# Optimization experiments

Measured on AMD Instinct MI355X. Metric: run time of the kernel, lower is better.

Reference implementation:

```python
import jax, jax.numpy as jnp
import numpy as np

B, S, DIM = 2, 2048, 2048
NH, HD, HDR = 16, 128, 64
DCKV, DCQ = 512, 1536


def _lin(x, W, b):
    return x @ W.T + b


def _rotate_half(x):
    x1, x2 = jnp.split(x, 2, axis=-1)
    return jnp.concatenate([-x2, x1], axis=-1)


def _rope(x, cos, sin):
    # x: [..., s, hdr]; cos/sin: [s, hdr]
    return x * cos + _rotate_half(x) * sin


def setup_inputs() -> dict:
    key = jax.random.key(0)
    ks = jax.random.split(key, 20)
    sc = 0.02

    def w(k, shape):
        return (jax.random.normal(k, shape, jnp.float32) * sc)

    inp = {}
    inp['x'] = jax.random.normal(ks[0], (B, S, DIM), jnp.float32)
    # standard RoPE tables for the decoupled rotary dim
    inv_freq = 1.0 / (10000.0 ** (jnp.arange(0, HDR, 2, dtype=jnp.float32) / HDR))
    t = jnp.arange(S, dtype=jnp.float32)
    freqs = jnp.outer(t, inv_freq)                      # [S, HDR/2]
    emb = jnp.concatenate([freqs, freqs], axis=-1)      # [S, HDR]
    inp['freq_cos'] = jnp.cos(emb)
    inp['freq_sin'] = jnp.sin(emb)
    inp['W_dq'] = w(ks[1], (DCQ, DIM));  inp['b_dq'] = jnp.zeros((DCQ,), jnp.float32)
    inp['W_uq'] = w(ks[2], (NH * HD, DCQ)); inp['b_uq'] = jnp.zeros((NH * HD,), jnp.float32)
    inp['W_qr'] = w(ks[3], (NH * HDR, DCQ)); inp['b_qr'] = jnp.zeros((NH * HDR,), jnp.float32)
    inp['W_dkv'] = w(ks[4], (DCKV, DIM)); inp['b_dkv'] = jnp.zeros((DCKV,), jnp.float32)
    inp['W_uk'] = w(ks[5], (NH * HD, DCKV)); inp['b_uk'] = jnp.zeros((NH * HD,), jnp.float32)
    inp['W_uv'] = w(ks[6], (NH * HD, DCKV)); inp['b_uv'] = jnp.zeros((NH * HD,), jnp.float32)
    inp['W_kr'] = w(ks[7], (HDR, DIM)); inp['b_kr'] = jnp.zeros((HDR,), jnp.float32)
    inp['W_out'] = w(ks[8], (DIM, DIM)); inp['b_out'] = jnp.zeros((DIM,), jnp.float32)
    return inp


def reference(x, freq_cos, freq_sin,
              W_dq, b_dq, W_uq, b_uq, W_qr, b_qr,
              W_dkv, b_dkv, W_uk, b_uk, W_uv, b_uv,
              W_kr, b_kr, W_out, b_out):
    b, s, d = x.shape
    c_q = _lin(x, W_dq, b_dq)                                  # [b,s,dcq]
    c_kv = _lin(x, W_dkv, b_dkv)                               # [b,s,dckv]
    c_q_r = _lin(c_q, W_qr, b_qr).reshape(b, s, NH, HDR).transpose(0, 2, 1, 3)  # [b,nh,s,hdr]
    k_r = _lin(x, W_kr, b_kr)[:, None]                         # [b,1,s,hdr]
    cos = freq_cos[:s]
    sin = freq_sin[:s]
    r_q = _rope(c_q_r, cos, sin)
    r_k = _rope(k_r, cos, sin)
    r_q = r_q.transpose(0, 2, 1, 3).reshape(b, s, NH * HDR)    # [b,s,nh*hdr]
    r_k = r_k[:, 0]                                            # [b,s,hdr]
    q = jnp.concatenate([_lin(c_q, W_uq, b_uq), r_q], axis=-1)  # [b,s,nh*hd+nh*hdr]
    k_base = _lin(c_kv, W_uk, b_uk)                            # [b,s,nh*hd]
    v = _lin(c_kv, W_uv, b_uv)                                 # [b,s,nh*hd]
    r_k_exp = jnp.broadcast_to(r_k[:, :, None, :], (b, s, NH, HDR)).reshape(b, s, NH * HDR)
    k = jnp.concatenate([k_base, r_k_exp], axis=-1)
    # faithful to original: view the concat into nh chunks of (hd+hdr)
    q = q.reshape(b, s, NH, HD + HDR).transpose(0, 2, 1, 3)    # [b,nh,s,hd+hdr]
    k = k.reshape(b, s, NH, HD + HDR).transpose(0, 2, 1, 3)
    v = v.reshape(b, s, NH, HD).transpose(0, 2, 1, 3)          # [b,nh,s,hd]
    scale = 1.0 / np.float32(np.sqrt(HD + HDR))
    att = jnp.einsum('bhqd,bhkd->bhqk', q, k) * scale          # [b,nh,s,s]
    mask = jnp.tril(jnp.ones((s, s), dtype=bool))
    att = jnp.where(mask, att, jnp.float32(-jnp.inf))
    att = jax.nn.softmax(att, axis=-1)
    y = jnp.einsum('bhqk,bhkd->bhqd', att, v)                  # [b,nh,s,hd]
    y = y.transpose(0, 2, 1, 3).reshape(b, s, d)
    return _lin(y, W_out, b_out)
```

## Files before the change

kernel.cpp:

```cpp
#include <hip/hip_runtime.h>
#include <hip/hip_bf16.h>
#include <stdint.h>


typedef __bf16 bf16x8 __attribute__((ext_vector_type(8)));
typedef float  f32x4  __attribute__((ext_vector_type(4)));

__device__ __forceinline__ uint16_t f2bf(float f) {
    uint32_t u = __builtin_bit_cast(uint32_t, f);
    u = (u + 0x7FFFu + ((u >> 16) & 1u)) >> 16;
    return (uint16_t)u;
}
__device__ __forceinline__ float bf2f(uint16_t h) {
    uint32_t u = ((uint32_t)h) << 16;
    return __builtin_bit_cast(float, u);
}

typedef __attribute__((address_space(3))) uint32_t lds_u32_t;
typedef const __attribute__((address_space(1))) uint32_t glb_u32_t;

__device__ __forceinline__ void gld16(const void* g, const void* l) {
    __builtin_amdgcn_global_load_lds((glb_u32_t*)(uintptr_t)g,
                                     (lds_u32_t*)(uint32_t)(uintptr_t)l, 16, 0, 0);
}

__global__ __launch_bounds__(256)
void conv_kernel(const float* __restrict__ src, uint16_t* __restrict__ dst,
                 int n_src, int n_dst)
{
    int i = (blockIdx.x * 256 + threadIdx.x) << 2;
    if (i >= n_dst) return;
    ushort4 o;
    if (i < n_src) {
        float4 v = *(const float4*)(src + i);
        o.x = f2bf(v.x); o.y = f2bf(v.y); o.z = f2bf(v.z); o.w = f2bf(v.w);
    } else {
        o.x = 0; o.y = 0; o.z = 0; o.w = 0;
    }
    *(ushort4*)(dst + i) = o;
}

template<int MODE>
__global__ __launch_bounds__(256, 2)
void gemm_fused(const uint16_t* __restrict__ A, const uint16_t* __restrict__ W,
                const float* __restrict__ b0, const float* __restrict__ b1,
                const float* __restrict__ b2,
                void* __restrict__ O0, void* __restrict__ O1,
                int M, int N, int K, int lda, int s1, int s2)
{
    __shared__ __align__(16) uint16_t Alds[128 * 32];
    __shared__ __align__(16) uint16_t Blds[128 * 32];

    const int tid  = threadIdx.x;
    const int lane = tid & 63;
    const int wave = tid >> 6;
    const int wm   = wave >> 1;
    const int wn   = wave & 1;
    const int m0   = blockIdx.y << 7;
    const int n0   = blockIdx.x << 7;

    f32x4 acc[4][4];
    #pragma unroll
    for (int i = 0; i < 4; ++i)
        #pragma unroll
        for (int j = 0; j < 4; ++j)
            acc[i][j] = (f32x4){0.f, 0.f, 0.f, 0.f};

    const int r0 = (wave << 5) + (lane >> 2);
    const int ck = (lane & 3) << 3;
    const uint16_t* gA0 = A + (size_t)(m0 + r0) * lda + ck;
    const uint16_t* gA1 = gA0 + (size_t)16 * lda;
    const uint16_t* gB0 = W + (size_t)(n0 + r0) * K + ck;
    const uint16_t* gB1 = gB0 + (size_t)16 * K;
    const uint16_t* lA0 = Alds + (wave << 10);
    const uint16_t* lA1 = lA0 + 512;
    const uint16_t* lB0 = Blds + (wave << 10);
    const uint16_t* lB1 = lB0 + 512;

    const int rsel = lane & 15;
    const int g8   = (lane >> 4) << 3;

    const int nK = K >> 5;
    for (int kt = 0; kt < nK; ++kt) {
        __syncthreads();
        gld16(gA0, lA0); gld16(gA1, lA1);
        gld16(gB0, lB0); gld16(gB1, lB1);
        gA0 += 32; gA1 += 32; gB0 += 32; gB1 += 32;
        __syncthreads();

        bf16x8 af[4], bfr[4];
        #pragma unroll
        for (int i = 0; i < 4; ++i)
            af[i] = *(const bf16x8*)&Alds[(((wm << 6) + (i << 4) + rsel) << 5) + g8];
        #pragma unroll
        for (int j = 0; j < 4; ++j)
            bfr[j] = *(const bf16x8*)&Blds[(((wn << 6) + (j << 4) + rsel) << 5) + g8];

        #pragma unroll
        for (int i = 0; i < 4; ++i)
            #pragma unroll
            for (int j = 0; j < 4; ++j)
                acc[i][j] = __builtin_amdgcn_mfma_f32_16x16x32_bf16(af[i], bfr[j], acc[i][j], 0, 0, 0);
    }

    const int col = lane & 15;
    const int rg  = lane >> 4;
    #pragma unroll
    for (int i = 0; i < 4; ++i) {
        #pragma unroll
        for (int j = 0; j < 4; ++j) {
            int n = n0 + (wn << 6) + (j << 4) + col;
            if (n >= N) continue;
            float bv = (n < s1) ? b0[n] : (n < s2) ? b1[n - s1] : b2[n - s2];
            float v[4];
            #pragma unroll
            for (int r = 0; r < 4; ++r) v[r] = acc[i][j][r] + bv;
            int mbase = m0 + (wm << 6) + (i << 4) + (rg << 2);
            if (MODE == 0) {
                uint16_t* o = (uint16_t*)O0 + (size_t)mbase * N + n;
                #pragma unroll
                for (int r = 0; r < 4; ++r) o[(size_t)r * N] = f2bf(v[r]);
            } else if (MODE == 3) {
                float* o = (float*)O0 + (size_t)mbase * N + n;
                #pragma unroll
                for (int r = 0; r < 4; ++r) o[(size_t)r * N] = v[r];
            } else {
                if (n < s1) {
                    int hh = n / 192, d = n - hh * 192;
                    int b = mbase >> 11, s = mbase & 2047;
                    uint16_t* o = (uint16_t*)O0 + (((size_t)(b * 16 + hh) * 2048 + s) * 192) + d;
                    #pragma unroll
                    for (int r = 0; r < 4; ++r) o[r * 192] = f2bf(v[r]);
                } else if (MODE == 4) {
                    int nn = n - s1;
                    uint16_t* o = (uint16_t*)O1 + (size_t)mbase * (N - s1) + nn;
                    #pragma unroll
                    for (int r = 0; r < 4; ++r) o[(size_t)r * (N - s1)] = f2bf(v[r]);
                } else {
                    int nn = n - s1;
                    int hh = nn >> 7, d = nn & 127;
                    int b = mbase >> 11, s = mbase & 2047;
                    ushort4 o4;
                    o4.x = f2bf(v[0]); o4.y = f2bf(v[1]); o4.z = f2bf(v[2]); o4.w = f2bf(v[3]);
                    *(ushort4*)&((uint16_t*)O1)[(((size_t)(b * 16 + hh) * 128 + d) * 2048) + s] = o4;
                }
            }
        }
    }
}

__global__ __launch_bounds__(256)
void rope_q_kernel(const uint16_t* __restrict__ raw, const float* __restrict__ fc,
                   const float* __restrict__ fs, uint16_t* __restrict__ qp)
{
    int gid = blockIdx.x * 256 + threadIdx.x;
    int m = gid >> 10, n = gid & 1023;
    int hh = n >> 6, d = n & 63;
    int b = m >> 11, s = m & 2047;
    float x  = bf2f(raw[(size_t)m * 1024 + n]);
    float xo = bf2f(raw[(size_t)m * 1024 + hh * 64 + ((d < 32) ? d + 32 : d - 32)]);
    float rot = (d < 32) ? -xo : xo;
    float v = x * fc[s * 64 + d] + rot * fs[s * 64 + d];
    int f = 2048 + n;
    int head = f / 192, dq = f - head * 192;
    qp[(((size_t)(b * 16 + head) * 2048 + s) * 192) + dq] = f2bf(v);
}

__global__ __launch_bounds__(256)
void rope_k_kernel(const uint16_t* __restrict__ raw, int ldr,
                   const float* __restrict__ fc, const float* __restrict__ fs,
                   uint16_t* __restrict__ kp)
{
    int gid = blockIdx.x * 256 + threadIdx.x;
    int m = gid >> 6, d = gid & 63;
    int b = m >> 11, s = m & 2047;
    float x  = bf2f(raw[(size_t)m * ldr + d]);
    float xo = bf2f(raw[(size_t)m * ldr + ((d < 32) ? d + 32 : d - 32)]);
    float rot = (d < 32) ? -xo : xo;
    uint16_t bv = f2bf(x * fc[s * 64 + d] + rot * fs[s * 64 + d]);
    #pragma unroll
    for (int hh = 0; hh < 16; ++hh) {
        int f = 2048 + hh * 64 + d;
        int head = f / 192, dk = f - head * 192;
        kp[(((size_t)(b * 16 + head) * 2048 + s) * 192) + dk] = bv;
    }
}

__global__ __launch_bounds__(256)
void attn_mfma3(const uint16_t* __restrict__ qp, const uint16_t* __restrict__ kp,
                const uint16_t* __restrict__ vt, uint16_t* __restrict__ yf)
{
    __shared__ uint16_t Ks[64][200];
    __shared__ uint16_t Vs[128][72];
    __shared__ uint16_t Ps[4][16][72];

    const int tid  = threadIdx.x;
    const int lane = tid & 63;
    const int w    = tid >> 6;
    const int g    = lane >> 4;
    const int li   = lane & 15;
    const int bh   = blockIdx.y;
    const int b    = bh >> 4;
    const int h    = bh & 15;

    const size_t qkb = (size_t)bh * 2048 * 192;
    const size_t vtb = (size_t)bh * 128 * 2048;
    const float scl = 0.07216878364870323f * 1.4426950408889634f;

    for (int pass = 0; pass < 2; ++pass) {
        const int jq = pass ? (int)blockIdx.x : 31 - (int)blockIdx.x;
        const int q0 = jq << 6;

        bf16x8 qf[6];
        #pragma unroll
        for (int kk = 0; kk < 6; ++kk)
            qf[kk] = *(const bf16x8*)(qp + qkb +
                (size_t)(q0 + (w << 4) + li) * 192 + kk * 32 + (g << 3));

        float mst[4], lst[4];
        f32x4 oacc[8];
        #pragma unroll
        for (int r = 0; r < 4; ++r) { mst[r] = -__builtin_inff(); lst[r] = 0.f; }
        #pragma unroll
        for (int ct = 0; ct < 8; ++ct) oacc[ct] = (f32x4){0.f, 0.f, 0.f, 0.f};

        for (int t = 0; t <= jq; ++t) {
            const int j0 = t << 6;
            __syncthreads();
            #pragma unroll
            for (int p = 0; p < 6; ++p) {
                int idx = tid + p * 256;
                int r = idx / 24, c8 = (idx - r * 24) << 3;
                *(bf16x8*)&Ks[r][c8] = *(const bf16x8*)(kp + qkb + (size_t)(j0 + r) * 192 + c8);
            }
            #pragma unroll
            for (int p = 0; p < 8; ++p) {
                int idx = tid + p * 256;
                int r = idx >> 4, c4 = (idx & 15) << 2;
                *(ushort4*)&Vs[r][c4] = *(const ushort4*)(vt + vtb + (size_t)r * 2048 + j0 + c4);
            }
            __syncthreads();

            f32x4 sacc[4];
            #pragma unroll
            for (int c = 0; c < 4; ++c) sacc[c] = (f32x4){0.f, 0.f, 0.f, 0.f};
            #pragma unroll
            for (int c = 0; c < 4; ++c) {
                #pragma unroll
                for (int kk = 0; kk < 6; ++kk) {
                    bf16x8 kf = *(const bf16x8*)&Ks[(c << 4) + li][kk * 32 + (g << 3)];
                    sacc[c] = __builtin_amdgcn_mfma_f32_16x16x32_bf16(qf[kk], kf, sacc[c], 0, 0, 0);
                }
            }

            float corr[4];
            #pragma unroll
            for (int r = 0; r < 4; ++r) {
                const int rq = q0 + (w << 4) + (g << 2) + r;
                float sv[4];
                float mx = -__builtin_inff();
                #pragma unroll
                for (int c = 0; c < 4; ++c) {
                    int colk = j0 + (c << 4) + li;
                    sv[c] = (colk <= rq) ? sacc[c][r] * scl : -__builtin_inff();
                    mx = fmaxf(mx, sv[c]);
                }
                #pragma unroll
                for (int off = 8; off >= 1; off >>= 1) mx = fmaxf(mx, __shfl_xor(mx, off, 64));
                float mnew = fmaxf(mst[r], mx);
                corr[r] = exp2f(mst[r] - mnew);
                mst[r] = mnew;
                float psum = 0.f;
                #pragma unroll
                for (int c = 0; c < 4; ++c) {
                    float p = exp2f(sv[c] - mnew);
                    psum += p;
                    Ps[w][(g << 2) + r][(c << 4) + li] = f2bf(p);
                }
                #pragma unroll
                for (int off = 8; off >= 1; off >>= 1) psum += __shfl_xor(psum, off, 64);
                lst[r] = lst[r] * corr[r] + psum;
            }

            #pragma unroll
            for (int ct = 0; ct < 8; ++ct)
                #pragma unroll
                for (int r = 0; r < 4; ++r) oacc[ct][r] *= corr[r];

            bf16x8 pf0 = *(const bf16x8*)&Ps[w][li][(g << 3)];
            bf16x8 pf1 = *(const bf16x8*)&Ps[w][li][32 + (g << 3)];
            #pragma unroll
            for (int ct = 0; ct < 8; ++ct) {
                bf16x8 vf0 = *(const bf16x8*)&Vs[(ct << 4) + li][(g << 3)];
                bf16x8 vf1 = *(const bf16x8*)&Vs[(ct << 4) + li][32 + (g << 3)];
                oacc[ct] = __builtin_amdgcn_mfma_f32_16x16x32_bf16(pf0, vf0, oacc[ct], 0, 0, 0);
                oacc[ct] = __builtin_amdgcn_mfma_f32_16x16x32_bf16(pf1, vf1, oacc[ct], 0, 0, 0);
            }
        }

        #pragma unroll
        for (int r = 0; r < 4; ++r) {
            float inv = 1.f / lst[r];
            int rq = q0 + (w << 4) + (g << 2) + r;
            size_t obase = ((size_t)(b * 2048 + rq) * 2048) + h * 128;
            #pragma unroll
            for (int ct = 0; ct < 8; ++ct)
                yf[obase + (ct << 4) + li] = f2bf(oacc[ct][r] * inv);
        }
    }
}

extern "C" void kernel_launch(void* const* d_in, const int* in_sizes, int n_in,
                              void* d_out, int out_size, void* d_ws, size_t ws_size,
                              hipStream_t stream)
{
    const float* x     = (const float*)d_in[0];
    const float* fcos  = (const float*)d_in[1];
    const float* fsin  = (const float*)d_in[2];
    const float* W_dq  = (const float*)d_in[3];
    const float* b_dq  = (const float*)d_in[4];
    const float* W_uq  = (const float*)d_in[5];
    const float* b_uq  = (const float*)d_in[6];
    const float* W_qr  = (const float*)d_in[7];
    const float* b_qr  = (const float*)d_in[8];
    const float* W_dkv = (const float*)d_in[9];
    const float* b_dkv = (const float*)d_in[10];
    const float* W_uk  = (const float*)d_in[11];
    const float* b_uk  = (const float*)d_in[12];
    const float* W_uv  = (const float*)d_in[13];
    const float* b_uv  = (const float*)d_in[14];
    const float* W_kr  = (const float*)d_in[15];
    const float* b_kr  = (const float*)d_in[16];
    const float* W_out = (const float*)d_in[17];
    const float* b_out = (const float*)d_in[18];

    char* ws = (char*)d_ws;
    uint16_t* xb     = (uint16_t*)(ws + 0);
    uint16_t* Wcat2  = (uint16_t*)(ws + 0);
    uint16_t* Wcat3  = (uint16_t*)(ws + 9437184);
    uint16_t* yf     = (uint16_t*)(ws + 0);
    uint16_t* Wout_b = (uint16_t*)(ws + 16777216);
    uint16_t* qp     = (uint16_t*)(ws + 25165824);
    uint16_t* kp     = (uint16_t*)(ws + 50331648);
    uint16_t* qr_raw = (uint16_t*)(ws + 50331648);
    uint16_t* vt     = (uint16_t*)(ws + 75497472);
    uint16_t* Wcat1  = (uint16_t*)(ws + 75497472);
    uint16_t* c_all  = (uint16_t*)(ws + 92274688);

    dim3 blk(256);
    conv_kernel<<<dim3(8192), blk, 0, stream>>>(x,     xb,                8388608, 8388608);
    conv_kernel<<<dim3(3072), blk, 0, stream>>>(W_dq,  Wcat1,             3145728, 3145728);
    conv_kernel<<<dim3(1024), blk, 0, stream>>>(W_dkv, Wcat1 + 3145728,   1048576, 1048576);
    conv_kernel<<<dim3( 256), blk, 0, stream>>>(W_kr,  Wcat1 + 4194304,    131072,  262144);
    conv_kernel<<<dim3(4096), blk, 0, stream>>>(W_out, Wout_b,            4194304, 4194304);

    gemm_fused<0><<<dim3(17, 32), blk, 0, stream>>>(
        xb, Wcat1, b_dq, b_dkv, b_kr, c_all, nullptr,
        4096, 2112, 2048, 2048, 1536, 2048);

    conv_kernel<<<dim3(3072), blk, 0, stream>>>(W_uq, Wcat2,             3145728, 3145728);
    conv_kernel<<<dim3(1536), blk, 0, stream>>>(W_qr, Wcat2 + 3145728,   1572864, 1572864);
    conv_kernel<<<dim3(1024), blk, 0, stream>>>(W_uk, Wcat3,             1048576, 1048576);
    conv_kernel<<<dim3(1024), blk, 0, stream>>>(W_uv, Wcat3 + 1048576,   1048576, 1048576);

    gemm_fused<4><<<dim3(24, 32), blk, 0, stream>>>(
        c_all, Wcat2, b_uq, b_qr, b_qr, qp, qr_raw,
        4096, 3072, 1536, 2112, 2048, 3072);

    rope_q_kernel<<<dim3(16384), blk, 0, stream>>>(qr_raw, fcos, fsin, qp);

    gemm_fused<5><<<dim3(32, 32), blk, 0, stream>>>(
        c_all + 1536, Wcat3, b_uk, b_uv, b_uv, kp, vt,
        4096, 4096, 512, 2112, 2048, 4096);

    rope_k_kernel<<<dim3(1024), blk, 0, stream>>>(c_all + 2048, 2112, fcos, fsin, kp);

    attn_mfma3<<<dim3(16, 32), blk, 0, stream>>>(qp, kp, vt, yf);

    gemm_fused<3><<<dim3(16, 32), blk, 0, stream>>>(
        yf, Wout_b, b_out, b_out, b_out, d_out, nullptr,
        4096, 2048, 2048, 2048, 2048, 2048);
}
```

Measured before the change: 362.2 us.

## Fuse query RoPE into GEMM epilogue and add lazy softmax rescaling in attention

The query-rotary GEMM epilogue now applies RoPE directly, taking the rotate-half partner from the accumulator tile at j^2 (32 columns away), and writes straight into the packed q buffer. This removes the separate rope_q kernel and its raw intermediate round-trip. The attention kernel restricts causal masking to the diagonal tile and skips max-reduction and output rescaling when a new tile's max stays within 8 (log2 units) of the running max, a lazy-rescale trick that trades some exp headroom for fewer shuffles and multiplies. It also raises wave priority around the MFMA sections with s_setprio.

```diff
diff --git a/kernel.cpp b/kernel.cpp
--- a/kernel.cpp
+++ b/kernel.cpp
@@ -45,6 +45,7 @@
 void gemm_fused(const uint16_t* __restrict__ A, const uint16_t* __restrict__ W,
                 const float* __restrict__ b0, const float* __restrict__ b1,
                 const float* __restrict__ b2,
+                const float* __restrict__ fc, const float* __restrict__ fs,
                 void* __restrict__ O0, void* __restrict__ O1,
                 int M, int N, int K, int lda, int s1, int s2)
 {
@@ -125,21 +126,30 @@
                 #pragma unroll
                 for (int r = 0; r < 4; ++r) o[(size_t)r * N] = v[r];
             } else {
+                int b = mbase >> 11, s = mbase & 2047;
                 if (n < s1) {
                     int hh = n / 192, d = n - hh * 192;
-                    int b = mbase >> 11, s = mbase & 2047;
                     uint16_t* o = (uint16_t*)O0 + (((size_t)(b * 16 + hh) * 2048 + s) * 192) + d;
                     #pragma unroll
                     for (int r = 0; r < 4; ++r) o[r * 192] = f2bf(v[r]);
                 } else if (MODE == 4) {
                     int nn = n - s1;
-                    uint16_t* o = (uint16_t*)O1 + (size_t)mbase * (N - s1) + nn;
-                    #pragma unroll
-                    for (int r = 0; r < 4; ++r) o[(size_t)r * (N - s1)] = f2bf(v[r]);
+                    int d  = nn & 63;
+                    float bp = b1[nn ^ 32];
+                    int f = 2048 + nn;
+                    int head = f / 192, dq = f - head * 192;
+                    uint16_t* o = (uint16_t*)O0 + (((size_t)(b * 16 + head) * 2048 + s) * 192) + dq;
+                    #pragma unroll
+                    for (int r = 0; r < 4; ++r) {
+                        float pv  = acc[i][j ^ 2][r] + bp;
+                        float rot = (d < 32) ? -pv : pv;
+                        int   sl  = s + r;
+                        float out = v[r] * fc[(size_t)sl * 64 + d] + rot * fs[(size_t)sl * 64 + d];
+                        o[r * 192] = f2bf(out);
+                    }
                 } else {
                     int nn = n - s1;
                     int hh = nn >> 7, d = nn & 127;
-                    int b = mbase >> 11, s = mbase & 2047;
                     ushort4 o4;
                     o4.x = f2bf(v[0]); o4.y = f2bf(v[1]); o4.z = f2bf(v[2]); o4.w = f2bf(v[3]);
                     *(ushort4*)&((uint16_t*)O1)[(((size_t)(b * 16 + hh) * 128 + d) * 2048) + s] = o4;
@@ -147,23 +157,6 @@
             }
         }
     }
-}
-
-__global__ __launch_bounds__(256)
-void rope_q_kernel(const uint16_t* __restrict__ raw, const float* __restrict__ fc,
-                   const float* __restrict__ fs, uint16_t* __restrict__ qp)
-{
-    int gid = blockIdx.x * 256 + threadIdx.x;
-    int m = gid >> 10, n = gid & 1023;
-    int hh = n >> 6, d = n & 63;
-    int b = m >> 11, s = m & 2047;
-    float x  = bf2f(raw[(size_t)m * 1024 + n]);
-    float xo = bf2f(raw[(size_t)m * 1024 + hh * 64 + ((d < 32) ? d + 32 : d - 32)]);
-    float rot = (d < 32) ? -xo : xo;
-    float v = x * fc[s * 64 + d] + rot * fs[s * 64 + d];
-    int f = 2048 + n;
-    int head = f / 192, dq = f - head * 192;
-    qp[(((size_t)(b * 16 + head) * 2048 + s) * 192) + dq] = f2bf(v);
 }
 
 __global__ __launch_bounds__(256)
@@ -187,7 +180,7 @@
 }
 
 __global__ __launch_bounds__(256)
-void attn_mfma3(const uint16_t* __restrict__ qp, const uint16_t* __restrict__ kp,
+void attn_mfma4(const uint16_t* __restrict__ qp, const uint16_t* __restrict__ kp,
                 const uint16_t* __restrict__ vt, uint16_t* __restrict__ yf)
 {
     __shared__ uint16_t Ks[64][200];
@@ -206,6 +199,7 @@
     const size_t qkb = (size_t)bh * 2048 * 192;
     const size_t vtb = (size_t)bh * 128 * 2048;
     const float scl = 0.07216878364870323f * 1.4426950408889634f;
+    const float NEGINF = -__builtin_inff();
 
     for (int pass = 0; pass < 2; ++pass) {
         const int jq = pass ? (int)blockIdx.x : 31 - (int)blockIdx.x;
@@ -220,7 +214,7 @@
         float mst[4], lst[4];
         f32x4 oacc[8];
         #pragma unroll
-        for (int r = 0; r < 4; ++r) { mst[r] = -__builtin_inff(); lst[r] = 0.f; }
+        for (int r = 0; r < 4; ++r) { mst[r] = NEGINF; lst[r] = 0.f; }
         #pragma unroll
         for (int ct = 0; ct < 8; ++ct) oacc[ct] = (f32x4){0.f, 0.f, 0.f, 0.f};
 
@@ -244,6 +238,7 @@
             f32x4 sacc[4];
             #pragma unroll
             for (int c = 0; c < 4; ++c) sacc[c] = (f32x4){0.f, 0.f, 0.f, 0.f};
+            __builtin_amdgcn_s_setprio(1);
             #pragma unroll
             for (int c = 0; c < 4; ++c) {
                 #pragma unroll
@@ -252,43 +247,73 @@
                     sacc[c] = __builtin_amdgcn_mfma_f32_16x16x32_bf16(qf[kk], kf, sacc[c], 0, 0, 0);
                 }
             }
-
-            float corr[4];
+            __builtin_amdgcn_s_setprio(0);
+
+            const bool diag = (t == jq);
+            float sv[4][4], mx4[4];
             #pragma unroll
             for (int r = 0; r < 4; ++r) {
-                const int rq = q0 + (w << 4) + (g << 2) + r;
-                float sv[4];
-                float mx = -__builtin_inff();
+                mx4[r] = NEGINF;
                 #pragma unroll
                 for (int c = 0; c < 4; ++c) {
-                    int colk = j0 + (c << 4) + li;
-                    sv[c] = (colk <= rq) ? sacc[c][r] * scl : -__builtin_inff();
-                    mx = fmaxf(mx, sv[c]);
+                    float s = sacc[c][r] * scl;
+                    if (diag) {
+                        int colk = j0 + (c << 4) + li;
+                        int rq = q0 + (w << 4) + (g << 2) + r;
+                        s = (colk <= rq) ? s : NEGINF;
+                    }
+                    sv[r][c] = s;
+                    mx4[r] = fmaxf(mx4[r], s);
                 }
-                #pragma unroll
-                for (int off = 8; off >= 1; off >>= 1) mx = fmaxf(mx, __shfl_xor(mx, off, 64));
-                float mnew = fmaxf(mst[r], mx);
-                corr[r] = exp2f(mst[r] - mnew);
-                mst[r] = mnew;
-                float psum = 0.f;
-                #pragma unroll
-                for (int c = 0; c < 4; ++c) {
-                    float p = exp2f(sv[c] - mnew);
-                    psum += p;
-                    Ps[w][(g << 2) + r][(c << 4) + li] = f2bf(p);
+            }
+
+            bool ok = true;
+            #pragma unroll
+            for (int r = 0; r < 4; ++r) ok = ok && (mx4[r] <= mst[r] + 8.f);
+            if (__all(ok)) {
+                #pragma unroll
+                for (int r = 0; r < 4; ++r) {
+                    float psum = 0.f;
+                    #pragma unroll
+                    for (int c = 0; c < 4; ++c) {
+                        float p = exp2f(sv[r][c] - mst[r]);
+                        psum += p;
+                        Ps[w][(g << 2) + r][(c << 4) + li] = f2bf(p);
+                    }
+                    #pragma unroll
+                    for (int off = 8; off >= 1; off >>= 1) psum += __shfl_xor(psum, off, 64);
+                    lst[r] += psum;
                 }
-                #pragma unroll
-                for (int off = 8; off >= 1; off >>= 1) psum += __shfl_xor(psum, off, 64);
-                lst[r] = lst[r] * corr[r] + psum;
-            }
-
-            #pragma unroll
-            for (int ct = 0; ct < 8; ++ct)
-                #pragma unroll
-                for (int r = 0; r < 4; ++r) oacc[ct][r] *= corr[r];
+            } else {
+                float corr[4];
+                #pragma unroll
+                for (int r = 0; r < 4; ++r) {
+                    float mx = mx4[r];
+                    #pragma unroll
+                    for (int off = 8; off >= 1; off >>= 1) mx = fmaxf(mx, __shfl_xor(mx, off, 64));
+                    float mnew = fmaxf(mst[r], mx);
+                    corr[r] = exp2f(mst[r] - mnew);
+                    mst[r] = mnew;
+                    float psum = 0.f;
+                    #pragma unroll
+                    for (int c = 0; c < 4; ++c) {
+                        float p = exp2f(sv[r][c] - mnew);
+                        psum += p;
+                        Ps[w][(g << 2) + r][(c << 4) + li] = f2bf(p);
+                    }
+                    #pragma unroll
+                    for (int off = 8; off >= 1; off >>= 1) psum += __shfl_xor(psum, off, 64);
+                    lst[r] = lst[r] * corr[r] + psum;
+                }
+                #pragma unroll
+                for (int ct = 0; ct < 8; ++ct)
+                    #pragma unroll
+                    for (int r = 0; r < 4; ++r) oacc[ct][r] *= corr[r];
+            }
 
             bf16x8 pf0 = *(const bf16x8*)&Ps[w][li][(g << 3)];
             bf16x8 pf1 = *(const bf16x8*)&Ps[w][li][32 + (g << 3)];
+            __builtin_amdgcn_s_setprio(1);
             #pragma unroll
             for (int ct = 0; ct < 8; ++ct) {
                 bf16x8 vf0 = *(const bf16x8*)&Vs[(ct << 4) + li][(g << 3)];
@@ -296,6 +321,7 @@
                 oacc[ct] = __builtin_amdgcn_mfma_f32_16x16x32_bf16(pf0, vf0, oacc[ct], 0, 0, 0);
                 oacc[ct] = __builtin_amdgcn_mfma_f32_16x16x32_bf16(pf1, vf1, oacc[ct], 0, 0, 0);
             }
+            __builtin_amdgcn_s_setprio(0);
         }
 
         #pragma unroll
@@ -342,7 +368,6 @@
     uint16_t* Wout_b = (uint16_t*)(ws + 16777216);
     uint16_t* qp     = (uint16_t*)(ws + 25165824);
     uint16_t* kp     = (uint16_t*)(ws + 50331648);
-    uint16_t* qr_raw = (uint16_t*)(ws + 50331648);
     uint16_t* vt     = (uint16_t*)(ws + 75497472);
     uint16_t* Wcat1  = (uint16_t*)(ws + 75497472);
     uint16_t* c_all  = (uint16_t*)(ws + 92274688);
@@ -355,7 +380,7 @@
     conv_kernel<<<dim3(4096), blk, 0, stream>>>(W_out, Wout_b,            4194304, 4194304);
 
     gemm_fused<0><<<dim3(17, 32), blk, 0, stream>>>(
-        xb, Wcat1, b_dq, b_dkv, b_kr, c_all, nullptr,
+        xb, Wcat1, b_dq, b_dkv, b_kr, nullptr, nullptr, c_all, nullptr,
         4096, 2112, 2048, 2048, 1536, 2048);
 
     conv_kernel<<<dim3(3072), blk, 0, stream>>>(W_uq, Wcat2,             3145728, 3145728);
@@ -364,20 +389,18 @@
     conv_kernel<<<dim3(1024), blk, 0, stream>>>(W_uv, Wcat3 + 1048576,   1048576, 1048576);
 
     gemm_fused<4><<<dim3(24, 32), blk, 0, stream>>>(
-        c_all, Wcat2, b_uq, b_qr, b_qr, qp, qr_raw,
+        c_all, Wcat2, b_uq, b_qr, b_qr, fcos, fsin, qp, nullptr,
         4096, 3072, 1536, 2112, 2048, 3072);
 
-    rope_q_kernel<<<dim3(16384), blk, 0, stream>>>(qr_raw, fcos, fsin, qp);
-
     gemm_fused<5><<<dim3(32, 32), blk, 0, stream>>>(
-        c_all + 1536, Wcat3, b_uk, b_uv, b_uv, kp, vt,
+        c_all + 1536, Wcat3, b_uk, b_uv, b_uv, nullptr, nullptr, kp, vt,
         4096, 4096, 512, 2112, 2048, 4096);
 
     rope_k_kernel<<<dim3(1024), blk, 0, stream>>>(c_all + 2048, 2112, fcos, fsin, kp);
 
-    attn_mfma3<<<dim3(16, 32), blk, 0, stream>>>(qp, kp, vt, yf);
+    attn_mfma4<<<dim3(16, 32), blk, 0, stream>>>(qp, kp, vt, yf);
 
     gemm_fused<3><<<dim3(16, 32), blk, 0, stream>>>(
-        yf, Wout_b, b_out, b_out, b_out, d_out, nullptr,
+        yf, Wout_b, b_out, b_out, b_out, nullptr, nullptr, d_out, nullptr,
         4096, 2048, 2048, 2048, 2048, 2048);
 }
```

Result: slower. 420.4 us (+16.1%).
